# Performance work log

Measured on AMD Instinct MI355X. Metric: run time of the kernel, lower is better.

Reference implementation:

```python
import jax, jax.numpy as jnp
import numpy as np
from jax import lax

C = 256
K = 3
KK = K * K
PAD = 1


def conv2d(x, w, b, pad):
    # x: [B,Cin,H,W], w: [Cout,Cin,kh,kw]
    y = lax.conv_general_dilated(x, w, (1, 1), [(pad, pad), (pad, pad)],
                                 dimension_numbers=("NCHW", "OIHW", "NCHW"))
    return y + b[None, :, None, None]


def _bilinear_gather(x, ys, xs):
    # x: [B,C,H,W]; ys, xs: [B,KK,H,W] float sample coords (pixel space).
    # Zero padding outside the image (torchvision deform_conv2d semantics).
    B, Cc, H, W = x.shape
    y0 = jnp.floor(ys)
    x0 = jnp.floor(xs)
    fy = ys - y0
    fx = xs - x0
    xf = x.reshape(B, Cc, H * W)

    def gather_b(xb, ib):
        return jnp.take(xb, ib, axis=1)  # [C, KK*H*W]

    out = jnp.zeros((B, Cc, KK, H, W), dtype=x.dtype)
    corners = [
        (y0, x0, (1 - fy) * (1 - fx)),
        (y0, x0 + 1, (1 - fy) * fx),
        (y0 + 1, x0, fy * (1 - fx)),
        (y0 + 1, x0 + 1, fy * fx),
    ]
    for yi, xi, wgt in corners:
        valid = (yi >= 0) & (yi < H) & (xi >= 0) & (xi < W)
        yc = jnp.clip(yi, 0, H - 1).astype(jnp.int32)
        xc = jnp.clip(xi, 0, W - 1).astype(jnp.int32)
        idx = (yc * W + xc).reshape(B, -1)  # [B, KK*H*W]
        g = jax.vmap(gather_b)(xf, idx).reshape(B, Cc, KK, H, W)
        out = out + g * (wgt * valid.astype(x.dtype))[:, None]
    return out


def deform_conv2d(x, offset, weight):
    # x: [B,C,H,W]; offset: [B, 2*KK, H, W] with layout (k, (dy, dx));
    # weight: [Cout, Cin, K, K]; stride 1, padding 1, no mask/bias.
    B, Cin, H, W = x.shape
    off = offset.reshape(B, KK, 2, H, W)
    dy = off[:, :, 0]  # [B,KK,H,W]
    dx = off[:, :, 1]
    ky = (jnp.arange(KK, dtype=x.dtype) // K) - PAD  # kernel row offsets
    kx = (jnp.arange(KK, dtype=x.dtype) % K) - PAD
    ys = dy + jnp.arange(H, dtype=x.dtype)[None, None, :, None] + ky[None, :, None, None]
    xs = dx + jnp.arange(W, dtype=x.dtype)[None, None, None, :] + kx[None, :, None, None]
    sampled = _bilinear_gather(x, ys, xs)  # [B,Cin,KK,H,W]
    Cout = weight.shape[0]
    return jnp.einsum("bckhw,ock->bohw", sampled, weight.reshape(Cout, Cin, KK))


def setup_inputs() -> dict:
    key = jax.random.key(0)
    ks = jax.random.split(key, 12)
    B, H, W = 2, 128, 128
    s = 0.05
    inp = {
        "ft_1": jax.random.normal(ks[0], (B, C, H, W), jnp.float32),
        "ft_2": jax.random.normal(ks[1], (B, C, H, W), jnp.float32),
        "ft_3": jax.random.normal(ks[2], (B, C, H, W), jnp.float32),
        "w1": jax.random.normal(ks[3], (256, 3 * C, 3, 3), jnp.float32) * s,
        "b1": jnp.zeros((256,), jnp.float32),
        "w2": jax.random.normal(ks[4], (256, 256, 3, 3), jnp.float32) * s,
        "b2": jnp.zeros((256,), jnp.float32),
        # last offset conv is zero-init in the original; use small random
        # values so the deformable sampling path is actually exercised
        "w3": jax.random.normal(ks[5], (2 * KK * 2, 256, 3, 3), jnp.float32) * 0.01,
        "b3": jax.random.normal(ks[6], (2 * KK * 2,), jnp.float32) * 0.01,
        "w_dcn2": jax.random.normal(ks[7], (C, C, 3, 3), jnp.float32) * s,
        "w_dcn3": jax.random.normal(ks[8], (C, C, 3, 3), jnp.float32) * s,
        "w_fuse": jax.random.normal(ks[9], (C, 3 * C, 1, 1), jnp.float32) * s,
        "b_fuse": jnp.zeros((C,), jnp.float32),
    }
    return inp


def reference(ft_1, ft_2, ft_3, w1, b1, w2, b2, w3, b3,
              w_dcn2, w_dcn3, w_fuse, b_fuse):
    combined = jnp.concatenate([ft_1, ft_2, ft_3], axis=1)  # [B,3C,H,W]
    h = jax.nn.relu(conv2d(combined, w1, b1, 1))
    h = jax.nn.relu(conv2d(h, w2, b2, 1))
    offsets_all = conv2d(h, w3, b3, 1)  # [B, 36, H, W]
    half = offsets_all.shape[1] // 2
    off_2 = offsets_all[:, :half]
    off_3 = offsets_all[:, half:]
    ft_2_aligned = deform_conv2d(ft_2, off_2, w_dcn2)
    ft_3_aligned = deform_conv2d(ft_3, off_3, w_dcn3)
    fused_raw = jnp.concatenate([ft_1, ft_2_aligned, ft_3_aligned], axis=1)
    return conv2d(fused_raw, w_fuse, b_fuse, 0)
```

## Files before the change

### kernel.cpp

```cpp
#include <hip/hip_runtime.h>
#include <stdint.h>

#define H_ 128
#define W_ 128
#define HW_ 16384
#define B_ 2
#define XP_ 130

typedef __attribute__((ext_vector_type(4))) float f32x4;
typedef _Float16 half_t;
typedef __attribute__((ext_vector_type(8))) _Float16 h8v;
typedef __attribute__((ext_vector_type(4))) _Float16 h4v;

__device__ __forceinline__ f32x4 MFMA(h8v a, h8v b, f32x4 c) {
  return __builtin_amdgcn_mfma_f32_16x16x32_f16(a, b, c, 0, 0, 0);
}
__device__ __forceinline__ f32x4 zero4() {
  f32x4 z; z[0] = 0.f; z[1] = 0.f; z[2] = 0.f; z[3] = 0.f; return z;
}
__device__ __forceinline__ h8v splat8(half_t x) {
  h8v v;
#pragma unroll
  for (int j = 0; j < 8; ++j) v[j] = x;
  return v;
}
__device__ __forceinline__ int swz(int r, int c8) {
  return r * 64 + ((c8 ^ (r & 7)) << 3);
}

template <int N>
__device__ __forceinline__ void s_wait_vmcnt() {
  asm volatile("s_waitcnt vmcnt(%0)" ::"n"(N) : "memory");
}

typedef const __attribute__((address_space(1))) uint32_t glb_u32;
typedef __attribute__((address_space(3))) uint32_t lds_u32;
__device__ __forceinline__ void gl_lds16(const half_t* g, half_t* l) {
  __builtin_amdgcn_global_load_lds((glb_u32*)(uintptr_t)g,
                                   (lds_u32*)(uint32_t)(uintptr_t)l, 16, 0, 0);
}

__global__ __launch_bounds__(256) void zeropad_all(
    half_t* __restrict__ xcat, half_t* __restrict__ h1p,
    half_t* __restrict__ h2p) {
  int idx = blockIdx.x * 256 + threadIdx.x;
  half_t* buf; int C, li;
  if (idx < 99072) { buf = xcat; C = 768; li = idx; }
  else if (idx < 132096) { buf = h1p; C = 256; li = idx - 99072; }
  else if (idx < 165120) { buf = h2p; C = 256; li = idx - 132096; }
  else return;
  int nc = C >> 3;
  int c8 = li % nc;
  int p = li / nc;
  int b = p / 516, i = p % 516;
  int y, x;
  if (i < 130) { y = 0; x = i; }
  else if (i < 260) { y = 129; x = i - 130; }
  else if (i < 388) { y = i - 260 + 1; x = 0; }
  else { y = i - 388 + 1; x = 129; }
  h8v z;
#pragma unroll
  for (int j = 0; j < 8; ++j) z[j] = (half_t)0.f;
  *(h8v*)(buf + ((size_t)(b * XP_ + y) * XP_ + x) * C + c8 * 8) = z;
}

__global__ __launch_bounds__(256) void pack_x(
    const float* __restrict__ f1, const float* __restrict__ f2,
    const float* __restrict__ f3, half_t* __restrict__ xcat) {
  __shared__ float tile[64][65];
  int bid = blockIdx.x;
  int t = bid % 24, by = bid / 24;
  int b = by >> 7, y = by & 127;
  int s = t / 8, t2 = t % 8;
  int x0 = (t2 & 1) * 64, c0 = (t2 >> 1) * 64;
  const float* f = (s == 0) ? f1 : ((s == 1) ? f2 : f3);
  int tid = threadIdx.x;
  int rx = tid & 63, rc = tid >> 6;
  const float* srcp = f + ((size_t)(b * 256 + c0)) * HW_ + (size_t)y * W_ + x0;
#pragma unroll
  for (int i = 0; i < 16; ++i) {
    int c = rc + i * 4;
    tile[c][rx] = srcp[(size_t)c * HW_ + rx];
  }
  __syncthreads();
#pragma unroll
  for (int it = 0; it < 2; ++it) {
    int task = tid + it * 256;
    int x = task & 63, c8 = task >> 6;
    h8v v;
#pragma unroll
    for (int j = 0; j < 8; ++j) v[j] = (half_t)tile[c8 * 8 + j][x];
    size_t pix = (size_t)(b * XP_ + y + 1) * XP_ + x0 + x + 1;
    *(h8v*)(xcat + pix * 768 + s * 256 + c0 + c8 * 8) = v;
  }
}

__device__ __forceinline__ void wt_conv(const float* __restrict__ w,
                                        half_t* __restrict__ wt, int CO, int CI,
                                        int idx) {
  int CS = CI >> 6;
  int e = idx & 8191, tile = idx >> 13;
  int task = e >> 3, j = e & 7;
  int r = task >> 3, c8 = (task & 7) ^ (r & 7);
  int tpb = 9 * CS;
  int coblk = tile / tpb, within = tile - coblk * tpb;
  int dx = within % 3, q = within / 3;
  int cs = q % CS, g = q / CS;
  int t = g * 3 + dx;
  int co = coblk * 128 + r;
  int ci = cs * 64 + c8 * 8 + j;
  float v = (co < CO) ? w[((size_t)co * CI + ci) * 9 + t] : 0.f;
  wt[idx] = (half_t)v;
}
__device__ __forceinline__ void wt_c64(const float* __restrict__ w,
                                       half_t* __restrict__ wt, int idx) {
  int e = idx & 4095, tile = idx >> 12;
  int task = e >> 3, j = e & 7;
  int r = task >> 3, c8 = (task & 7) ^ (r & 7);
  int dx = tile % 3, q = tile / 3;
  int cs = q & 3, g = q >> 2;
  int t = g * 3 + dx;
  int ci = cs * 64 + c8 * 8 + j;
  float v = (r < 36) ? w[((size_t)r * 256 + ci) * 9 + t] : 0.f;
  wt[idx] = (half_t)v;
}
__device__ __forceinline__ void wt_256(const float* __restrict__ w,
                                       half_t* __restrict__ wt, int idx) {
  int e = idx & 16383, tile = idx >> 14;
  int task = e >> 3, j = e & 7;
  int r = task >> 3, c8 = (task & 7) ^ (r & 7);
  int cs = tile & 3, t = tile >> 2;
  int ci = cs * 64 + c8 * 8 + j;
  wt[idx] = (half_t)w[((size_t)r * 256 + ci) * 9 + t];
}
__device__ __forceinline__ void wt_fuse(const float* __restrict__ w,
                                        half_t* __restrict__ wt, int idx) {
  int e = idx & 8191, tile = idx >> 13;
  int task = e >> 3, j = e & 7;
  int r = task >> 3, c8 = (task & 7) ^ (r & 7);
  int cs = tile % 12, coblk = tile / 12;
  int co = coblk * 128 + r;
  int ci = cs * 64 + c8 * 8 + j;
  wt[idx] = (half_t)w[(size_t)co * 768 + ci];
}

__global__ __launch_bounds__(256) void wtrans_all(
    const float* __restrict__ w1, half_t* __restrict__ w1t,
    const float* __restrict__ w2, half_t* __restrict__ w2t,
    const float* __restrict__ w3, half_t* __restrict__ w3t,
    const float* __restrict__ wd2, half_t* __restrict__ wd2t,
    const float* __restrict__ wd3, half_t* __restrict__ wd3t,
    const float* __restrict__ wf, half_t* __restrict__ wft) {
  int bid = blockIdx.x, tid = threadIdx.x;
  if (bid < 6912)       wt_conv(w1, w1t, 256, 768, bid * 256 + tid);
  else if (bid < 9216)  wt_conv(w2, w2t, 256, 256, (bid - 6912) * 256 + tid);
  else if (bid < 9792)  wt_c64(w3, w3t, (bid - 9216) * 256 + tid);
  else if (bid < 12096) wt_256(wd2, wd2t, (bid - 9792) * 256 + tid);
  else if (bid < 14400) wt_256(wd3, wd3t, (bid - 12096) * 256 + tid);
  else                  wt_fuse(wf, wft, (bid - 14400) * 256 + tid);
}

template <int CIN, bool RELU>
__global__ __launch_bounds__(256) void conv3x3(
    const half_t* __restrict__ in, const half_t* __restrict__ wt,
    const float* __restrict__ bias, half_t* __restrict__ outb) {
  constexpr int CS = CIN / 64;
  constexpr int NGI = 3 * CS;
  __shared__ __align__(16) half_t wl[2][8192];
  __shared__ __align__(16) half_t al[2][8704];
  int tid = threadIdx.x;
  int by = blockIdx.x;
  int b = by >> 7, y = by & 127;
  int co0 = blockIdx.y * 128;
  int w = tid >> 6, l = tid & 63, lr = l & 15, lg = l >> 4;
  int wr = (w >> 1) * 64, wc = (w & 1) * 64;
  f32x4 acc[4][4];
#pragma unroll
  for (int i = 0; i < 4; ++i)
#pragma unroll
    for (int j = 0; j < 4; ++j) acc[i][j] = zero4();

  const half_t* wbase = wt + (size_t)blockIdx.y * (9 * CS) * 8192;

  int ldsoff[4], aoff[4], ldsoff4, aoff4;
#pragma unroll
  for (int it = 0; it < 4; ++it) {
    int task = tid + it * 256;
    ldsoff[it] = task * 8;
    int r = task >> 3, c8 = (task & 7) ^ (r & 7);
    aoff[it] = r * CIN + c8 * 8;
  }
  {
    int task = 1024 + tid;
    ldsoff4 = task * 8;
    int r = task >> 3, c8 = (task & 7) ^ (r & 7);
    aoff4 = r * CIN + c8 * 8;
  }

  auto stage_w = [&](int s, int buf) {
    const half_t* wp = wbase + (size_t)s * 8192;
#pragma unroll
    for (int it = 0; it < 4; ++it)
      gl_lds16(wp + ldsoff[it], &wl[buf][ldsoff[it]]);
  };
  auto stage_a = [&](int gi, int buf) {
    int g = gi / CS, cs = gi - g * CS;
    const half_t* ap = in + ((size_t)(b * XP_ + y + g) * XP_) * CIN + cs * 64;
    if (tid < 64) gl_lds16(ap + aoff4, &al[buf][ldsoff4]);
#pragma unroll
    for (int it = 0; it < 4; ++it)
      gl_lds16(ap + aoff[it], &al[buf][ldsoff[it]]);
  };
  auto compute = [&](int dx, int wbuf, int abuf) {
    const half_t* wb = wl[wbuf];
    const half_t* ab = al[abuf];
    h8v af[4][2], bf[4][2];
#pragma unroll
    for (int cg = 0; cg < 4; ++cg)
#pragma unroll
      for (int kc = 0; kc < 2; ++kc)
        af[cg][kc] = *(const h8v*)(wb + swz(wr + 16 * cg + lr, 4 * kc + lg));
#pragma unroll
    for (int pg = 0; pg < 4; ++pg)
#pragma unroll
      for (int kc = 0; kc < 2; ++kc)
        bf[pg][kc] = *(const h8v*)(ab + swz(wc + 16 * pg + lr + dx, 4 * kc + lg));
    __builtin_amdgcn_s_setprio(1);
#pragma unroll
    for (int cg = 0; cg < 4; ++cg)
#pragma unroll
      for (int pg = 0; pg < 4; ++pg) {
        acc[cg][pg] = MFMA(af[cg][0], bf[pg][0], acc[cg][pg]);
        acc[cg][pg] = MFMA(af[cg][1], bf[pg][1], acc[cg][pg]);
      }
    __builtin_amdgcn_s_setprio(0);
  };

  stage_w(0, 0);
  stage_a(0, 0);
  for (int gi = 0; gi < NGI; ++gi) {
    int abuf = gi & 1;
    int s0 = 3 * gi;
    stage_w(s0 + 1, (s0 + 1) & 1);
    s_wait_vmcnt<4>();
    __builtin_amdgcn_s_barrier();
    compute(0, s0 & 1, abuf);
    __builtin_amdgcn_s_barrier();
    stage_w(s0 + 2, s0 & 1);
    s_wait_vmcnt<4>();
    __builtin_amdgcn_s_barrier();
    compute(1, (s0 + 1) & 1, abuf);
    __builtin_amdgcn_s_barrier();
    if (gi + 1 < NGI) {
      stage_w(s0 + 3, (s0 + 3) & 1);
      stage_a(gi + 1, abuf ^ 1);
      s_wait_vmcnt<8>();
    } else {
      s_wait_vmcnt<0>();
    }
    __builtin_amdgcn_s_barrier();
    compute(2, s0 & 1, abuf);
    __builtin_amdgcn_s_barrier();
  }
#pragma unroll
  for (int cg = 0; cg < 4; ++cg) {
    int co = co0 + wr + 16 * cg + 4 * lg;
    f32x4 bv = *(const f32x4*)(bias + co);
#pragma unroll
    for (int pg = 0; pg < 4; ++pg) {
      int px = wc + 16 * pg + lr;
      f32x4 v = acc[cg][pg];
#pragma unroll
      for (int r = 0; r < 4; ++r) {
        v[r] += bv[r];
        if (RELU) v[r] = fmaxf(v[r], 0.f);
      }
      size_t pix = (size_t)(b * XP_ + y + 1) * XP_ + px + 1;
      h4v pv;
#pragma unroll
      for (int r = 0; r < 4; ++r) pv[r] = (half_t)v[r];
      *(h4v*)(outb + pix * 256 + co) = pv;
    }
  }
}

__global__ __launch_bounds__(256) void conv3_c64(
    const half_t* __restrict__ in, const half_t* __restrict__ wt,
    const float* __restrict__ bias, float* __restrict__ outf) {
  constexpr int CIN = 256, CS = 4, NGI = 12;
  __shared__ __align__(16) half_t wl[2][4096];
  __shared__ __align__(16) half_t al[2][8704];
  int tid = threadIdx.x;
  int by = blockIdx.x;
  int b = by >> 7, y = by & 127;
  int w = tid >> 6, l = tid & 63, lr = l & 15, lg = l >> 4;
  int wc = w * 32;
  f32x4 acc[4][2];
#pragma unroll
  for (int i = 0; i < 4; ++i)
#pragma unroll
    for (int j = 0; j < 2; ++j) acc[i][j] = zero4();

  int ldsW[2];
#pragma unroll
  for (int it = 0; it < 2; ++it) ldsW[it] = (tid + it * 256) * 8;
  int ldsoff[4], aoff[4], ldsoff4, aoff4;
#pragma unroll
  for (int it = 0; it < 4; ++it) {
    int task = tid + it * 256;
    ldsoff[it] = task * 8;
    int r = task >> 3, c8 = (task & 7) ^ (r & 7);
    aoff[it] = r * CIN + c8 * 8;
  }
  {
    int task = 1024 + tid;
    ldsoff4 = task * 8;
    int r = task >> 3, c8 = (task & 7) ^ (r & 7);
    aoff4 = r * CIN + c8 * 8;
  }

  auto stage_w = [&](int s, int buf) {
    const half_t* wp = wt + (size_t)s * 4096;
#pragma unroll
    for (int it = 0; it < 2; ++it)
      gl_lds16(wp + ldsW[it], &wl[buf][ldsW[it]]);
  };
  auto stage_a = [&](int gi, int buf) {
    int g = gi / CS, cs = gi - g * CS;
    const half_t* ap = in + ((size_t)(b * XP_ + y + g) * XP_) * CIN + cs * 64;
    if (tid < 64) gl_lds16(ap + aoff4, &al[buf][ldsoff4]);
#pragma unroll
    for (int it = 0; it < 4; ++it)
      gl_lds16(ap + aoff[it], &al[buf][ldsoff[it]]);
  };
  auto compute = [&](int dx, int wbuf, int abuf) {
    const half_t* wb = wl[wbuf];
    const half_t* ab = al[abuf];
    h8v af[4][2], bf[2][2];
#pragma unroll
    for (int cg = 0; cg < 4; ++cg)
#pragma unroll
      for (int kc = 0; kc < 2; ++kc)
        af[cg][kc] = *(const h8v*)(wb + swz(16 * cg + lr, 4 * kc + lg));
#pragma unroll
    for (int pg = 0; pg < 2; ++pg)
#pragma unroll
      for (int kc = 0; kc < 2; ++kc)
        bf[pg][kc] = *(const h8v*)(ab + swz(wc + 16 * pg + lr + dx, 4 * kc + lg));
    __builtin_amdgcn_s_setprio(1);
#pragma unroll
    for (int cg = 0; cg < 4; ++cg)
#pragma unroll
      for (int pg = 0; pg < 2; ++pg) {
        acc[cg][pg] = MFMA(af[cg][0], bf[pg][0], acc[cg][pg]);
        acc[cg][pg] = MFMA(af[cg][1], bf[pg][1], acc[cg][pg]);
      }
    __builtin_amdgcn_s_setprio(0);
  };

  stage_w(0, 0);
  stage_a(0, 0);
  for (int gi = 0; gi < NGI; ++gi) {
    int abuf = gi & 1;
    int s0 = 3 * gi;
    stage_w(s0 + 1, (s0 + 1) & 1);
    s_wait_vmcnt<2>();
    __builtin_amdgcn_s_barrier();
    compute(0, s0 & 1, abuf);
    __builtin_amdgcn_s_barrier();
    stage_w(s0 + 2, s0 & 1);
    s_wait_vmcnt<2>();
    __builtin_amdgcn_s_barrier();
    compute(1, (s0 + 1) & 1, abuf);
    __builtin_amdgcn_s_barrier();
    if (gi + 1 < NGI) {
      stage_w(s0 + 3, (s0 + 3) & 1);
      stage_a(gi + 1, abuf ^ 1);
      s_wait_vmcnt<6>();
    } else {
      s_wait_vmcnt<0>();
    }
    __builtin_amdgcn_s_barrier();
    compute(2, s0 & 1, abuf);
    __builtin_amdgcn_s_barrier();
  }
#pragma unroll
  for (int cg = 0; cg < 4; ++cg) {
    int co = 16 * cg + 4 * lg;
    if (co >= 36) continue;
    f32x4 bv = *(const f32x4*)(bias + co);
#pragma unroll
    for (int pg = 0; pg < 2; ++pg) {
      int px = wc + 16 * pg + lr;
      f32x4 v = acc[cg][pg];
#pragma unroll
      for (int r = 0; r < 4; ++r) v[r] += bv[r];
      size_t pix = (size_t)(b * H_ + y) * W_ + px;
      *(f32x4*)(outf + pix * 36 + co) = v;
    }
  }
}

__global__ __launch_bounds__(512) void dcn(
    const half_t* __restrict__ xcat, const float* __restrict__ off,
    const half_t* __restrict__ wt2, const half_t* __restrict__ wt3,
    half_t* __restrict__ out2, half_t* __restrict__ out3) {
  __shared__ __align__(16) half_t wl[2][16384];
  __shared__ __align__(16) half_t al[2][8192];
  __shared__ int caddr[2][128][4];
  __shared__ half_t chw[2][128][4];
  int gy = blockIdx.y;
  const half_t* wt = gy ? wt3 : wt2;
  half_t* outb = gy ? out3 : out2;
  int cbase = 256 + (gy << 8);
  int obase = 18 * gy;
  int tid = threadIdx.x;
  int bx = blockIdx.x;
  int by = ((bx & 7) << 5) | (bx >> 3);
  int b = by >> 7, y = by & 127;
  int w = tid >> 6, l = tid & 63, lr = l & 15, lg = l >> 4;
  int wr = (w >> 1) * 64, wc = (w & 1) * 64;
  size_t rowpix = (size_t)(b * H_ + y) * W_;
  f32x4 acc[4][4];
#pragma unroll
  for (int i = 0; i < 4; ++i)
#pragma unroll
    for (int j = 0; j < 4; ++j) acc[i][j] = zero4();

  auto coeffs = [&](int t) {
    if (tid < 128) {
      int px = tid;
      const float* op = off + (rowpix + px) * 36 + obase + 2 * t;
      float dy = op[0], dx = op[1];
      float ysf = (float)(y + (t / 3) - 1) + dy;
      float xsf = (float)(px + (t % 3) - 1) + dx;
      float y0f = floorf(ysf), x0f = floorf(xsf);
      float fy = ysf - y0f, fx = xsf - x0f;
      int y0 = (int)y0f, x0 = (int)x0f;
#pragma unroll
      for (int c = 0; c < 4; ++c) {
        int iy = y0 + (c >> 1), ix = x0 + (c & 1);
        float wc2 = ((c >> 1) ? fy : 1.f - fy) * ((c & 1) ? fx : 1.f - fx);
        bool valid = (iy >= 0) && (iy < H_) && (ix >= 0) && (ix < W_);
        int cy = iy < 0 ? 0 : (iy > H_ - 1 ? H_ - 1 : iy);
        int cx = ix < 0 ? 0 : (ix > W_ - 1 ? W_ - 1 : ix);
        caddr[t & 1][px][c] = ((b * XP_ + cy + 1) * XP_ + cx + 1) * 768 + cbase;
        chw[t & 1][px][c] = (half_t)(valid ? wc2 : 0.f);
      }
    }
  };

  h8v cv[2][4];
  auto blendload = [&](int s) {
    int t = (s >> 2) & 1;
    int c0 = (s & 3) * 64;
#pragma unroll
    for (int it = 0; it < 2; ++it) {
      int task = tid + it * 512;
      int px = task >> 3;
      int cc = c0 + (task & 7) * 8;
#pragma unroll
      for (int c = 0; c < 4; ++c)
        cv[it][c] = *(const h8v*)(xcat + caddr[t][px][c] + cc);
    }
  };
  auto blendwrite = [&](int s, int buf) {
    int t = (s >> 2) & 1;
#pragma unroll
    for (int it = 0; it < 2; ++it) {
      int task = tid + it * 512;
      int px = task >> 3, c8 = task & 7;
      h8v av = cv[it][0] * splat8(chw[t][px][0]);
      av += cv[it][1] * splat8(chw[t][px][1]);
      av += cv[it][2] * splat8(chw[t][px][2]);
      av += cv[it][3] * splat8(chw[t][px][3]);
      *(h8v*)(&al[buf][swz(px, c8)]) = av;
    }
  };
  auto stagew = [&](int s, int buf) {
    const half_t* wp = wt + (size_t)s * 16384;
#pragma unroll
    for (int it = 0; it < 4; ++it) {
      int task = tid + it * 512;
      gl_lds16(wp + task * 8, &wl[buf][task * 8]);
    }
  };

  coeffs(0);
  __syncthreads();
  stagew(0, 0);
  blendload(0);
  blendwrite(0, 0);
  __syncthreads();
  for (int s = 0; s < 36; ++s) {
    int cur = s & 1, nxt = cur ^ 1;
    if (s + 1 < 36) {
      stagew(s + 1, nxt);
      blendload(s + 1);
    }
    if ((s & 3) == 0 && (s >> 2) + 1 < 9) coeffs((s >> 2) + 1);
    const half_t* wb = wl[cur];
    const half_t* ab = al[cur];
    h8v af[4][2], bf[4][2];
#pragma unroll
    for (int cg = 0; cg < 4; ++cg)
#pragma unroll
      for (int kc = 0; kc < 2; ++kc)
        af[cg][kc] = *(const h8v*)(wb + swz(wr + 16 * cg + lr, 4 * kc + lg));
#pragma unroll
    for (int pg = 0; pg < 4; ++pg)
#pragma unroll
      for (int kc = 0; kc < 2; ++kc)
        bf[pg][kc] = *(const h8v*)(ab + swz(wc + 16 * pg + lr, 4 * kc + lg));
    __builtin_amdgcn_s_setprio(1);
#pragma unroll
    for (int cg = 0; cg < 4; ++cg)
#pragma unroll
      for (int pg = 0; pg < 4; ++pg) {
        acc[cg][pg] = MFMA(af[cg][0], bf[pg][0], acc[cg][pg]);
        acc[cg][pg] = MFMA(af[cg][1], bf[pg][1], acc[cg][pg]);
      }
    __builtin_amdgcn_s_setprio(0);
    if (s + 1 < 36) blendwrite(s + 1, nxt);
    __syncthreads();
  }
#pragma unroll
  for (int cg = 0; cg < 4; ++cg) {
    int co = wr + 16 * cg + 4 * lg;
#pragma unroll
    for (int pg = 0; pg < 4; ++pg) {
      int px = wc + 16 * pg + lr;
      size_t pix = rowpix + px;
      f32x4 v = acc[cg][pg];
      h4v pv;
#pragma unroll
      for (int r = 0; r < 4; ++r) pv[r] = (half_t)v[r];
      *(h4v*)(outb + pix * 256 + co) = pv;
    }
  }
}

__global__ __launch_bounds__(256) void fuse1x1(
    const half_t* __restrict__ xcat, const half_t* __restrict__ al2,
    const half_t* __restrict__ al3, const half_t* __restrict__ wt,
    const float* __restrict__ bias, float* __restrict__ out) {
  __shared__ __align__(16) half_t wl[2][8192];
  __shared__ __align__(16) half_t al[2][8192];
  int tid = threadIdx.x;
  int by = blockIdx.x;
  int b = by >> 7, y = by & 127;
  int co0 = blockIdx.y * 128;
  int w = tid >> 6, l = tid & 63, lr = l & 15, lg = l >> 4;
  int pxb = (w >> 1) * 64, cob = (w & 1) * 64;
  f32x4 acc[4][4];
#pragma unroll
  for (int i = 0; i < 4; ++i)
#pragma unroll
    for (int j = 0; j < 4; ++j) acc[i][j] = zero4();

  const half_t* wbase = wt + (size_t)blockIdx.y * 12 * 8192;
  size_t rowpix = (size_t)(b * H_ + y) * W_;
  const half_t* xrow = xcat + ((size_t)(b * XP_ + y + 1) * XP_ + 1) * 768;

  int woff[4], rr[4], c8x8[4];
#pragma unroll
  for (int it = 0; it < 4; ++it) {
    int task = tid + it * 256;
    woff[it] = task * 8;
    rr[it] = task >> 3;
    c8x8[it] = (((task & 7) ^ (rr[it] & 7))) * 8;
  }

  auto stage = [&](int cs, int buf) {
    const half_t* wp = wbase + (size_t)cs * 8192;
#pragma unroll
    for (int it = 0; it < 4; ++it) gl_lds16(wp + woff[it], &wl[buf][woff[it]]);
#pragma unroll
    for (int it = 0; it < 4; ++it) {
      int kk = cs * 64 + c8x8[it];
      const half_t* sp;
      if (kk < 256) sp = xrow + (size_t)rr[it] * 768 + kk;
      else if (kk < 512) sp = al2 + (rowpix + rr[it]) * 256 + (kk - 256);
      else sp = al3 + (rowpix + rr[it]) * 256 + (kk - 512);
      gl_lds16(sp, &al[buf][woff[it]]);
    }
  };

  stage(0, 0);
  for (int cs = 0; cs < 12; ++cs) {
    int cur = cs & 1;
    if (cs + 1 < 12) {
      stage(cs + 1, cur ^ 1);
      s_wait_vmcnt<8>();
    } else {
      s_wait_vmcnt<0>();
    }
    __builtin_amdgcn_s_barrier();
    const half_t* wb = wl[cur];
    const half_t* ab = al[cur];
    h8v af[4][2], bf[4][2];
#pragma unroll
    for (int pg = 0; pg < 4; ++pg)
#pragma unroll
      for (int kc = 0; kc < 2; ++kc)
        af[pg][kc] = *(const h8v*)(ab + swz(pxb + 16 * pg + lr, 4 * kc + lg));
#pragma unroll
    for (int cg = 0; cg < 4; ++cg)
#pragma unroll
      for (int kc = 0; kc < 2; ++kc)
        bf[cg][kc] = *(const h8v*)(wb + swz(cob + 16 * cg + lr, 4 * kc + lg));
    __builtin_amdgcn_s_setprio(1);
#pragma unroll
    for (int pg = 0; pg < 4; ++pg)
#pragma unroll
      for (int cg = 0; cg < 4; ++cg) {
        acc[pg][cg] = MFMA(af[pg][0], bf[cg][0], acc[pg][cg]);
        acc[pg][cg] = MFMA(af[pg][1], bf[cg][1], acc[pg][cg]);
      }
    __builtin_amdgcn_s_setprio(0);
    __builtin_amdgcn_s_barrier();
  }
#pragma unroll
  for (int pg = 0; pg < 4; ++pg)
#pragma unroll
    for (int cg = 0; cg < 4; ++cg) {
      int px = pxb + 16 * pg + 4 * lg;
      int co = co0 + cob + 16 * cg + lr;
      float bb = bias[co];
      f32x4 v = acc[pg][cg];
#pragma unroll
      for (int r = 0; r < 4; ++r) v[r] += bb;
      *(f32x4*)(out + ((size_t)(b * 256 + co)) * HW_ + (size_t)y * W_ + px) = v;
    }
}

extern "C" void kernel_launch(void* const* d_in, const int* in_sizes, int n_in,
                              void* d_out, int out_size, void* d_ws, size_t ws_size,
                              hipStream_t stream) {
  (void)in_sizes; (void)n_in; (void)out_size; (void)ws_size;
  const float* ft1 = (const float*)d_in[0];
  const float* ft2 = (const float*)d_in[1];
  const float* ft3 = (const float*)d_in[2];
  const float* w1 = (const float*)d_in[3];
  const float* b1 = (const float*)d_in[4];
  const float* w2 = (const float*)d_in[5];
  const float* b2 = (const float*)d_in[6];
  const float* w3 = (const float*)d_in[7];
  const float* b3 = (const float*)d_in[8];
  const float* wd2 = (const float*)d_in[9];
  const float* wd3 = (const float*)d_in[10];
  const float* wf = (const float*)d_in[11];
  const float* bfu = (const float*)d_in[12];

  char* p = (char*)d_ws;
  half_t* xcat = (half_t*)p; p += (size_t)B_ * XP_ * XP_ * 768 * 2;
  half_t* h1p = (half_t*)p;  p += (size_t)B_ * XP_ * XP_ * 256 * 2;
  half_t* h2p = (half_t*)p;  p += (size_t)B_ * XP_ * XP_ * 256 * 2;
  float* off = (float*)p;    p += (size_t)B_ * HW_ * 36 * 4;
  half_t* w1t = (half_t*)p;  p += (size_t)2 * 9 * 12 * 8192 * 2;
  half_t* w2t = (half_t*)p;  p += (size_t)2 * 9 * 4 * 8192 * 2;
  half_t* w3t = (half_t*)p;  p += (size_t)36 * 4096 * 2;
  half_t* wd2t = (half_t*)p; p += (size_t)36 * 16384 * 2;
  half_t* wd3t = (half_t*)p; p += (size_t)36 * 16384 * 2;
  half_t* wft = (half_t*)p;  p += (size_t)2 * 12 * 8192 * 2;
  half_t* al2 = h1p;
  half_t* al3 = h2p;

  zeropad_all<<<645, 256, 0, stream>>>(xcat, h1p, h2p);
  pack_x<<<24 * B_ * H_, 256, 0, stream>>>(ft1, ft2, ft3, xcat);
  wtrans_all<<<15168, 256, 0, stream>>>(w1, w1t, w2, w2t, w3, w3t,
                                        wd2, wd2t, wd3, wd3t, wf, wft);

  conv3x3<768, true><<<dim3(B_ * H_, 2), 256, 0, stream>>>(xcat, w1t, b1, h1p);
  conv3x3<256, true><<<dim3(B_ * H_, 2), 256, 0, stream>>>(h1p, w2t, b2, h2p);
  conv3_c64<<<dim3(B_ * H_), 256, 0, stream>>>(h2p, w3t, b3, off);
  dcn<<<dim3(B_ * H_, 2), 512, 0, stream>>>(xcat, off, wd2t, wd3t, al2, al3);
  fuse1x1<<<dim3(B_ * H_, 2), 256, 0, stream>>>(xcat, al2, al3, wft, bfu, (float*)d_out);
}
```

Before: 332.5 us.

## Precompute all DCN tap coefficients upfront and deepen gather pipeline with fine-grained vmcnt waits

After: 321.1 us (median of 2 runs). -3.4%, faster.

```diff
diff --git a/kernel.cpp b/kernel.cpp
--- a/kernel.cpp
+++ b/kernel.cpp
@@ -407,8 +407,8 @@
     half_t* __restrict__ out2, half_t* __restrict__ out3) {
   __shared__ __align__(16) half_t wl[2][16384];
   __shared__ __align__(16) half_t al[2][8192];
-  __shared__ int caddr[2][128][4];
-  __shared__ half_t chw[2][128][4];
+  __shared__ int caddr[9][128][4];
+  __shared__ half_t chw[9][128][4];
   int gy = blockIdx.y;
   const half_t* wt = gy ? wt3 : wt2;
   half_t* outb = gy ? out3 : out2;
@@ -427,32 +427,30 @@
 #pragma unroll
     for (int j = 0; j < 4; ++j) acc[i][j] = zero4();
 
-  auto coeffs = [&](int t) {
-    if (tid < 128) {
-      int px = tid;
-      const float* op = off + (rowpix + px) * 36 + obase + 2 * t;
-      float dy = op[0], dx = op[1];
-      float ysf = (float)(y + (t / 3) - 1) + dy;
-      float xsf = (float)(px + (t % 3) - 1) + dx;
-      float y0f = floorf(ysf), x0f = floorf(xsf);
-      float fy = ysf - y0f, fx = xsf - x0f;
-      int y0 = (int)y0f, x0 = (int)x0f;
-#pragma unroll
-      for (int c = 0; c < 4; ++c) {
-        int iy = y0 + (c >> 1), ix = x0 + (c & 1);
-        float wc2 = ((c >> 1) ? fy : 1.f - fy) * ((c & 1) ? fx : 1.f - fx);
-        bool valid = (iy >= 0) && (iy < H_) && (ix >= 0) && (ix < W_);
-        int cy = iy < 0 ? 0 : (iy > H_ - 1 ? H_ - 1 : iy);
-        int cx = ix < 0 ? 0 : (ix > W_ - 1 ? W_ - 1 : ix);
-        caddr[t & 1][px][c] = ((b * XP_ + cy + 1) * XP_ + cx + 1) * 768 + cbase;
-        chw[t & 1][px][c] = (half_t)(valid ? wc2 : 0.f);
-      }
-    }
-  };
-
-  h8v cv[2][4];
-  auto blendload = [&](int s) {
-    int t = (s >> 2) & 1;
+  for (int e = tid; e < 1152; e += 512) {
+    int t = e >> 7, px = e & 127;
+    const float* op = off + (rowpix + px) * 36 + obase + 2 * t;
+    float dy = op[0], dx = op[1];
+    float ysf = (float)(y + (t / 3) - 1) + dy;
+    float xsf = (float)(px + (t % 3) - 1) + dx;
+    float y0f = floorf(ysf), x0f = floorf(xsf);
+    float fy = ysf - y0f, fx = xsf - x0f;
+    int y0 = (int)y0f, x0 = (int)x0f;
+#pragma unroll
+    for (int c = 0; c < 4; ++c) {
+      int iy = y0 + (c >> 1), ix = x0 + (c & 1);
+      float wc2 = ((c >> 1) ? fy : 1.f - fy) * ((c & 1) ? fx : 1.f - fx);
+      bool valid = (iy >= 0) && (iy < H_) && (ix >= 0) && (ix < W_);
+      int cy = iy < 0 ? 0 : (iy > H_ - 1 ? H_ - 1 : iy);
+      int cx = ix < 0 ? 0 : (ix > W_ - 1 ? W_ - 1 : ix);
+      caddr[t][px][c] = ((b * XP_ + cy + 1) * XP_ + cx + 1) * 768 + cbase;
+      chw[t][px][c] = (half_t)(valid ? wc2 : 0.f);
+    }
+  }
+  __syncthreads();
+
+  auto blendload = [&](int s, h8v (&cv)[2][4]) {
+    int t = s >> 2;
     int c0 = (s & 3) * 64;
 #pragma unroll
     for (int it = 0; it < 2; ++it) {
@@ -464,8 +462,8 @@
         cv[it][c] = *(const h8v*)(xcat + caddr[t][px][c] + cc);
     }
   };
-  auto blendwrite = [&](int s, int buf) {
-    int t = (s >> 2) & 1;
+  auto blendwrite = [&](int s, int buf, h8v (&cv)[2][4]) {
+    int t = s >> 2;
 #pragma unroll
     for (int it = 0; it < 2; ++it) {
       int task = tid + it * 512;
@@ -485,22 +483,7 @@
       gl_lds16(wp + task * 8, &wl[buf][task * 8]);
     }
   };
-
-  coeffs(0);
-  __syncthreads();
-  stagew(0, 0);
-  blendload(0);
-  blendwrite(0, 0);
-  __syncthreads();
-  for (int s = 0; s < 36; ++s) {
-    int cur = s & 1, nxt = cur ^ 1;
-    if (s + 1 < 36) {
-      stagew(s + 1, nxt);
-      blendload(s + 1);
-    }
-    if ((s & 3) == 0 && (s >> 2) + 1 < 9) coeffs((s >> 2) + 1);
-    const half_t* wb = wl[cur];
-    const half_t* ab = al[cur];
+  auto gemm_step = [&](const half_t* wb, const half_t* ab) {
     h8v af[4][2], bf[4][2];
 #pragma unroll
     for (int cg = 0; cg < 4; ++cg)
@@ -521,8 +504,31 @@
         acc[cg][pg] = MFMA(af[cg][1], bf[pg][1], acc[cg][pg]);
       }
     __builtin_amdgcn_s_setprio(0);
-    if (s + 1 < 36) blendwrite(s + 1, nxt);
-    __syncthreads();
+  };
+
+  h8v cvA[2][4], cvB[2][4];
+  stagew(0, 0);
+  blendload(0, cvA);
+  blendwrite(0, 0, cvA);
+  blendload(1, cvB);
+  __syncthreads();
+
+  for (int ss = 0; ss < 18; ++ss) {
+    int s0 = 2 * ss;
+    stagew(s0 + 1, 1);
+    if (s0 + 2 < 36) blendload(s0 + 2, cvA);
+    gemm_step(wl[0], al[0]);
+    blendwrite(s0 + 1, 1, cvB);
+    if (s0 + 2 < 36) s_wait_vmcnt<8>(); else s_wait_vmcnt<0>();
+    __builtin_amdgcn_s_barrier();
+
+    int s1 = s0 + 1;
+    if (s1 + 1 < 36) stagew(s1 + 1, 0);
+    if (s1 + 2 < 36) blendload(s1 + 2, cvB);
+    gemm_step(wl[1], al[1]);
+    if (s1 + 1 < 36) blendwrite(s1 + 1, 0, cvA);
+    if (s1 + 2 < 36) s_wait_vmcnt<8>(); else s_wait_vmcnt<0>();
+    __builtin_amdgcn_s_barrier();
   }
 #pragma unroll
   for (int cg = 0; cg < 4; ++cg) {
```
